# Optimization experiments

Hardware: AMD Instinct MI355X
Metric: run time of the kernel (lower is better)

## Reference

```python
import jax, jax.numpy as jnp
import numpy as np
from jax import lax

# ---- dims ----
B, L, DM = 4, 1024, 512          # batch, seq_len, model_dimension
NLAYERS = 6
EXPAND, HEADDIM, NSTATE, DCONV = 2, 64, 16, 4   # Mamba2 defaults; d_state = hidden_state_dim
DI = EXPAND * DM                 # d_inner = 1024
NH = DI // HEADDIM               # nheads = 16
CONV_DIM = DI + 2 * NSTATE       # x,B,C channels through depthwise conv = 1056
DPROJ = 2 * DI + 2 * NSTATE + NH # in_proj output width = 2096
DFF = 2048
EPS = 1e-5


def rmsnorm(x, w):
    return x * lax.rsqrt(jnp.mean(x * x, axis=-1, keepdims=True) + EPS) * w


def setup_inputs() -> dict:
    key = jax.random.key(0)
    ks = jax.random.split(key, 10)
    s = 0.02
    Ly = NLAYERS
    return {
        "x": jax.random.normal(ks[0], (B, L, DM), jnp.float32),
        "in_proj_w": jax.random.normal(ks[1], (Ly, DPROJ, DM), jnp.float32) * s,
        "conv_w": jax.random.normal(ks[2], (Ly, CONV_DIM, DCONV), jnp.float32) * s,
        "conv_b": jnp.zeros((Ly, CONV_DIM), jnp.float32),
        "dt_bias": jax.random.normal(ks[3], (Ly, NH), jnp.float32) * 0.5,
        "A_log": jnp.log(jax.random.uniform(ks[4], (Ly, NH), jnp.float32, 1.0, 16.0)),
        "D_ssm": jnp.ones((Ly, NH), jnp.float32),
        "gnorm_w": jnp.ones((Ly, DI), jnp.float32),
        "out_proj_w": jax.random.normal(ks[5], (Ly, DM, DI), jnp.float32) * s,
        "ffn_w1": jax.random.normal(ks[6], (Ly, DFF, DM), jnp.float32) * s,
        "ffn_b1": jnp.zeros((Ly, DFF), jnp.float32),
        "ffn_w2": jax.random.normal(ks[7], (Ly, DM, DFF), jnp.float32) * s,
        "ffn_b2": jnp.zeros((Ly, DM), jnp.float32),
        "norm_mamba_w": jnp.ones((Ly, DM), jnp.float32),
        "norm_ffn_w": jnp.ones((Ly, DM), jnp.float32),
        "final_norm_w": jnp.ones((DM,), jnp.float32),
    }


def _mamba2(u, Wp, cw, cb, dtb, Alog, Dh, gw, Wo):
    b, l, _ = u.shape
    zxbcdt = u @ Wp.T                                  # [b,l,DPROJ]
    z = zxbcdt[..., :DI]                               # gate
    xBC = zxbcdt[..., DI:DI + CONV_DIM]
    dt = jax.nn.softplus(zxbcdt[..., -NH:] + dtb)      # [b,l,H]
    # causal depthwise conv1d over time
    conv = lax.conv_general_dilated(
        xBC.transpose(0, 2, 1), cw[:, None, :], (1,), [(DCONV - 1, 0)],
        feature_group_count=CONV_DIM)
    xBC = jax.nn.silu(conv.transpose(0, 2, 1) + cb)
    xh = xBC[..., :DI].reshape(b, l, NH, HEADDIM)      # [b,l,H,P]
    Bm = xBC[..., DI:DI + NSTATE]                      # [b,l,N]
    Cm = xBC[..., DI + NSTATE:]                        # [b,l,N]
    dA = jnp.exp(dt * (-jnp.exp(Alog)))                # [b,l,H]

    def step(h, inp):
        xt, Bt, Ct, dAt, dtt = inp                     # [b,H,P],[b,N],[b,N],[b,H],[b,H]
        h = h * dAt[:, :, None, None] + (dtt[:, :, None] * xt)[..., None] * Bt[:, None, None, :]
        return h, jnp.einsum('bhpn,bn->bhp', h, Ct)

    h0 = jnp.zeros((b, NH, HEADDIM, NSTATE), u.dtype)
    xs = tuple(jnp.moveaxis(a, 1, 0) for a in (xh, Bm, Cm, dA, dt))
    _, ys = lax.scan(step, h0, xs)                     # ys: [l,b,H,P]
    y = jnp.moveaxis(ys, 0, 1) + Dh[None, None, :, None] * xh
    y = y.reshape(b, l, DI)
    y = rmsnorm(y * jax.nn.silu(z), gw)                # RMSNormGated
    return y @ Wo.T


def reference(x, in_proj_w, conv_w, conv_b, dt_bias, A_log, D_ssm, gnorm_w,
              out_proj_w, ffn_w1, ffn_b1, ffn_w2, ffn_b2,
              norm_mamba_w, norm_ffn_w, final_norm_w):
    for i in range(NLAYERS):
        res = x
        xn = rmsnorm(x, norm_mamba_w[i])
        x = _mamba2(xn, in_proj_w[i], conv_w[i], conv_b[i], dt_bias[i],
                    A_log[i], D_ssm[i], gnorm_w[i], out_proj_w[i]) + res
        res = x
        xn = rmsnorm(x, norm_ffn_w[i])
        h = jax.nn.gelu(xn @ ffn_w1[i].T + ffn_b1[i], approximate=False)
        x = h @ ffn_w2[i].T + ffn_b2[i] + res
    return rmsnorm(x, final_norm_w)
```

## Files before the change

### kernel.cpp

```cpp
#include <hip/hip_runtime.h>
#include <hip/hip_bf16.h>

#define NLAYERS 6
#define B_ 4
#define L_ 1024
#define DM_ 512
#define DI_ 1024
#define NH_ 16
#define HD_ 64
#define NS_ 16
#define CONVD_ 1056
#define DPROJ_ 2096
#define DFF_ 2048
#define ROWS_ (B_*L_)
#define EPS_ 1e-5f
#define NCHUNK_ 16
#define CLEN_ 64

typedef __bf16 bfx8 __attribute__((ext_vector_type(8)));
typedef float f32x4 __attribute__((ext_vector_type(4)));

typedef unsigned int u32_t;
typedef __attribute__((address_space(1))) const u32_t gu32_t;
typedef __attribute__((address_space(3))) u32_t lu32_t;

__device__ __forceinline__ void gload16(const __bf16* g, __bf16* l){
    __builtin_amdgcn_global_load_lds((gu32_t*)g, (lu32_t*)l, 16, 0, 0);
}

__device__ __forceinline__ float block_reduce_sum(float v){
    __shared__ float sm[8];
    #pragma unroll
    for (int off = 32; off > 0; off >>= 1) v += __shfl_xor(v, off);
    int lane = threadIdx.x & 63, wid = threadIdx.x >> 6;
    if (lane == 0) sm[wid] = v;
    __syncthreads();
    if (threadIdx.x == 0){
        float t = 0.f;
        int nw = blockDim.x >> 6;
        for (int i = 0; i < nw; i++) t += sm[i];
        sm[0] = t;
    }
    __syncthreads();
    return sm[0];
}

__global__ void copy_kernel(const float* __restrict__ x, float* __restrict__ X, int n){
    int i = blockIdx.x * blockDim.x + threadIdx.x;
    if (i < n) X[i] = x[i];
}

__global__ __launch_bounds__(64) void rowscale_kernel(const float* __restrict__ X,
                                                      float* __restrict__ rs){
    int row = blockIdx.x, lane = threadIdx.x;
    const float* xr = X + (size_t)row * DM_;
    float ss = 0.f;
    #pragma unroll
    for (int i = 0; i < DM_ / 64; i++){ float v = xr[lane + 64 * i]; ss += v * v; }
    #pragma unroll
    for (int off = 32; off > 0; off >>= 1) ss += __shfl_xor(ss, off);
    if (lane == 0) rs[row] = rsqrtf(ss / (float)DM_ + EPS_);
}

__global__ void finalnorm_kernel(const float* __restrict__ in, const float* __restrict__ w,
                                 float* __restrict__ out){
    int row = blockIdx.x;
    const float* xr = in + (size_t)row * DM_;
    float ss = 0.f;
    for (int c = threadIdx.x; c < DM_; c += blockDim.x){ float v = xr[c]; ss += v * v; }
    float tot = block_reduce_sum(ss);
    float rsv = rsqrtf(tot / (float)DM_ + EPS_);
    float* orow = out + (size_t)row * DM_;
    for (int c = threadIdx.x; c < DM_; c += blockDim.x)
        orow[c] = xr[c] * rsv * w[c];
}

__global__ void convA_kernel(const float* __restrict__ X, int lda,
                             const float* __restrict__ rs, const float* __restrict__ wv,
                             __bf16* __restrict__ A2, int M, int K){
    int idx = blockIdx.x * blockDim.x + threadIdx.x;
    if (idx >= M * K) return;
    int m = idx / K, k = idx - m * K;
    float a = X[(size_t)m * lda + k];
    if (rs) a *= rs[m];
    if (wv) a *= wv[k];
    __bf16 hi = (__bf16)a;
    A2[(size_t)m * (2 * K) + k] = hi;
    A2[(size_t)m * (2 * K) + K + k] = (__bf16)(a - (float)hi);
}

__global__ void convW_kernel(const float* __restrict__ W, __bf16* __restrict__ W2,
                             int N, int Npad, int K){
    int idx = blockIdx.x * blockDim.x + threadIdx.x;
    if (idx >= Npad * K) return;
    int n = idx / K, k = idx - n * K;
    size_t ro = (size_t)n * (3 * K);
    if (n >= N){
        W2[ro + k] = (__bf16)0.f; W2[ro + K + k] = (__bf16)0.f; W2[ro + 2 * K + k] = (__bf16)0.f;
        return;
    }
    float w = W[(size_t)n * K + k];
    __bf16 hi = (__bf16)w;
    __bf16 lo = (__bf16)(w - (float)hi);
    W2[ro + k] = hi; W2[ro + K + k] = lo; W2[ro + 2 * K + k] = hi;
}

__global__ void reduceK_kernel(const float* __restrict__ P, const float* __restrict__ bias,
                               float* __restrict__ X, int MN){
    int i = blockIdx.x * blockDim.x + threadIdx.x;
    if (i * 4 >= MN) return;
    float4 a = reinterpret_cast<const float4*>(P)[i];
    float4 b = reinterpret_cast<const float4*>(P + MN)[i];
    float4 x = reinterpret_cast<const float4*>(X)[i];
    float4 r;
    r.x = x.x + a.x + b.x; r.y = x.y + a.y + b.y;
    r.z = x.z + a.z + b.z; r.w = x.w + a.w + b.w;
    if (bias){
        int n = (i * 4) & (DM_ - 1);
        r.x += bias[n]; r.y += bias[n + 1]; r.z += bias[n + 2]; r.w += bias[n + 3];
    }
    reinterpret_cast<float4*>(X)[i] = r;
}

template<int BM, int BN>
__global__ __launch_bounds__(256, 3) void gemm_mfma_kernel(
    const __bf16* __restrict__ A2, const __bf16* __restrict__ W2,
    const float* __restrict__ bias, const float* __restrict__ resid, int ldr,
    float* __restrict__ Pf,
    float* __restrict__ Cf, int ldc, __bf16* __restrict__ Cs, int csK,
    int M, int N, int K, int act)
{
    constexpr int NI  = BM / 32;
    constexpr int NJ  = BN / 32;
    constexpr int NLD = (BM + BN) / 64;
    __shared__ __attribute__((aligned(16))) __bf16 As[3][BM * 32];
    __shared__ __attribute__((aligned(16))) __bf16 Ws[3][BN * 32];
    int tid = threadIdx.x;
    int m0 = blockIdx.x * BM, n0 = blockIdx.y * BN;
    int wv = tid >> 6, lane = tid & 63;
    int wm = (wv >> 1) * (BM / 2);
    int wn = (wv & 1) * (BN / 2);
    int lm = lane & 15, quad = lane >> 4;
    int soff = ((quad ^ ((lm >> 1) & 3)) * 8);
    const int ldA = 2 * K, ldW = 3 * K;
    const int nt = (3 * K) / 32;
    const int ntl = nt / gridDim.z;
    const int tb = blockIdx.z * ntl;

    f32x4 acc[NI][NJ] = {};

    auto stage = [&](int buf, int t){
        int k0 = t * 32;
        int ak0 = (k0 < K) ? k0 : (k0 - K);
        #pragma unroll
        for (int u = 0; u < BM / 64; u++){
            int cb = (wv * (BM / 64) + u) * 64;
            int c = cb + lane;
            int r = c >> 2, s = c & 3, q = s ^ ((r >> 1) & 3);
            gload16(A2 + (size_t)(m0 + r) * ldA + ak0 + q * 8, &As[buf][cb * 8]);
        }
        #pragma unroll
        for (int u = 0; u < BN / 64; u++){
            int cb = (wv * (BN / 64) + u) * 64;
            int c = cb + lane;
            int r = c >> 2, s = c & 3, q = s ^ ((r >> 1) & 3);
            gload16(W2 + (size_t)(n0 + r) * ldW + k0 + q * 8, &Ws[buf][cb * 8]);
        }
    };

    stage(0, tb);
    stage(1, tb + 1);
    if constexpr (NLD == 4)      asm volatile("s_waitcnt vmcnt(4)" ::: "memory");
    else if constexpr (NLD == 3) asm volatile("s_waitcnt vmcnt(3)" ::: "memory");
    else                         asm volatile("s_waitcnt vmcnt(2)" ::: "memory");
    __builtin_amdgcn_s_barrier();

    int cur = 0;
    for (int tt = 0; tt < ntl; tt++){
        bool staged = (tt + 2 < ntl);
        if (staged){
            int nb = cur + 2; if (nb >= 3) nb -= 3;
            stage(nb, tb + tt + 2);
        }

        bfx8 af[NI], bfr[NJ];
        #pragma unroll
        for (int i = 0; i < NI; i++)
            af[i] = *reinterpret_cast<const bfx8*>(&As[cur][(wm + i * 16 + lm) * 32 + soff]);
        #pragma unroll
        for (int j = 0; j < NJ; j++)
            bfr[j] = *reinterpret_cast<const bfx8*>(&Ws[cur][(wn + j * 16 + lm) * 32 + soff]);

        __builtin_amdgcn_s_setprio(1);
        #pragma unroll
        for (int i = 0; i < NI; i++)
            #pragma unroll
            for (int j = 0; j < NJ; j++)
                acc[i][j] = __builtin_amdgcn_mfma_f32_16x16x32_bf16(
                    af[i], bfr[j], acc[i][j], 0, 0, 0);
        __builtin_amdgcn_s_setprio(0);

        if (staged){
            if constexpr (NLD == 4)      asm volatile("s_waitcnt vmcnt(4)" ::: "memory");
            else if constexpr (NLD == 3) asm volatile("s_waitcnt vmcnt(3)" ::: "memory");
            else                         asm volatile("s_waitcnt vmcnt(2)" ::: "memory");
        } else {
            asm volatile("s_waitcnt vmcnt(0)" ::: "memory");
        }
        __builtin_amdgcn_s_barrier();
        cur = cur + 1; if (cur >= 3) cur = 0;
    }

    if (Pf){
        float* pc = Pf + (size_t)blockIdx.z * M * N;
        #pragma unroll
        for (int i = 0; i < NI; i++)
            #pragma unroll
            for (int j = 0; j < NJ; j++){
                int n = n0 + wn + j * 16 + lm;
                #pragma unroll
                for (int r = 0; r < 4; r++){
                    int m = m0 + wm + i * 16 + quad * 4 + r;
                    pc[(size_t)m * N + n] = acc[i][j][r];
                }
            }
        return;
    }

    #pragma unroll
    for (int i = 0; i < NI; i++){
        #pragma unroll
        for (int j = 0; j < NJ; j++){
            int n = n0 + wn + j * 16 + lm;
            if (n < N){
                #pragma unroll
                for (int r = 0; r < 4; r++){
                    int m = m0 + wm + i * 16 + quad * 4 + r;
                    float c = acc[i][j][r];
                    if (bias) c += bias[n];
                    if (act == 1) c = 0.5f * c * (1.f + erff(c * 0.70710678118654752f));
                    if (resid) c += resid[(size_t)m * ldr + n];
                    if (Cf) Cf[(size_t)m * ldc + n] = c;
                    else {
                        __bf16 hi = (__bf16)c;
                        Cs[(size_t)m * (2 * csK) + n] = hi;
                        Cs[(size_t)m * (2 * csK) + csK + n] = (__bf16)(c - (float)hi);
                    }
                }
            }
        }
    }
}

__global__ void bcconv_kernel(const float* __restrict__ ZX, const float* __restrict__ cw,
                              const float* __restrict__ cb, float* __restrict__ BCc){
    int idx = blockIdx.x * blockDim.x + threadIdx.x;
    if (idx >= ROWS_ * 32) return;
    int j = idx & 31;
    int row = idx >> 5;
    int l = row & (L_ - 1);
    float acc = cb[DI_ + j];
    #pragma unroll
    for (int k = 0; k < 4; k++){
        int lt = l + k - 3;
        if (lt >= 0)
            acc += ZX[(size_t)(row + k - 3) * DPROJ_ + (DI_ + DI_) + j] * cw[(DI_ + j) * 4 + k];
    }
    BCc[idx] = acc / (1.f + expf(-acc));
}

__global__ void dt_kernel(const float* __restrict__ ZX, const float* __restrict__ dtb,
                          const float* __restrict__ Alog, float* __restrict__ DT,
                          float* __restrict__ DA){
    int idx = blockIdx.x * blockDim.x + threadIdx.x;
    if (idx >= ROWS_ * NH_) return;
    int h = idx & 15; int row = idx >> 4;
    float v = ZX[(size_t)row * DPROJ_ + (DPROJ_ - NH_) + h] + dtb[h];
    float dtv = (v > 20.f) ? v : log1pf(expf(v));
    DT[idx] = dtv;
    DA[idx] = expf(-expf(Alog[h]) * dtv);
}

__global__ __launch_bounds__(64) void scanA_kernel(const float* __restrict__ ZX,
                                                   const float* __restrict__ BCc,
                                                   const float* __restrict__ DT,
                                                   const float* __restrict__ DA,
                                                   const float* __restrict__ cw,
                                                   const float* __restrict__ cb,
                                                   float* __restrict__ SCH,
                                                   float* __restrict__ PCH,
                                                   float* __restrict__ XWIN){
    int blk = blockIdx.x;
    int c = blk & (NCHUNK_ - 1); int h = (blk >> 4) & (NH_ - 1); int b = blk >> 8;
    int p = threadIdx.x;
    int ch = h * HD_ + p;
    float cw0 = cw[ch * 4 + 0], cw1 = cw[ch * 4 + 1], cw2 = cw[ch * 4 + 2], cw3 = cw[ch * 4 + 3];
    float cbc = cb[ch];
    size_t colx = (size_t)DI_ + ch;
    int t0 = c * CLEN_;
    float w0 = 0.f, w1 = 0.f, w2 = 0.f;
    if (c > 0){
        w0 = ZX[(size_t)(b * L_ + t0 - 3) * DPROJ_ + colx];
        w1 = ZX[(size_t)(b * L_ + t0 - 2) * DPROJ_ + colx];
        w2 = ZX[(size_t)(b * L_ + t0 - 1) * DPROJ_ + colx];
    }
    float* xw = XWIN + (size_t)blk * (3 * 64);
    xw[0 * 64 + p] = w0; xw[1 * 64 + p] = w1; xw[2 * 64 + p] = w2;

    float s[16];
    #pragma unroll
    for (int n = 0; n < 16; n++) s[n] = 0.f;
    float pprod = 1.f;

    for (int tt = 0; tt < CLEN_; tt++){
        int row = b * L_ + t0 + tt;
        size_t rowoff = (size_t)row * DPROJ_;
        float cur = ZX[rowoff + colx];
        float pre = cbc + cw0 * w0 + cw1 * w1 + cw2 * w2 + cw3 * cur;
        float xc = pre / (1.f + expf(-pre));
        w0 = w1; w1 = w2; w2 = cur;
        float dtv = DT[row * NH_ + h];
        float dav = DA[row * NH_ + h];
        pprod *= dav;
        float bc[16];
        const float4* bp = reinterpret_cast<const float4*>(BCc + (size_t)row * 32);
        #pragma unroll
        for (int i = 0; i < 4; i++){
            float4 v = bp[i];
            bc[4 * i + 0] = v.x; bc[4 * i + 1] = v.y; bc[4 * i + 2] = v.z; bc[4 * i + 3] = v.w;
        }
        float coef = dtv * xc;
        #pragma unroll
        for (int n = 0; n < 16; n++)
            s[n] = fmaf(s[n], dav, coef * bc[n]);
    }
    float* sc = SCH + (size_t)blk * 1024 + p * 16;
    #pragma unroll
    for (int i = 0; i < 4; i++)
        *reinterpret_cast<float4*>(sc + 4 * i) = make_float4(s[4*i], s[4*i+1], s[4*i+2], s[4*i+3]);
    if (p == 0) PCH[blk] = pprod;
}

__global__ __launch_bounds__(64) void scanB_kernel(float* __restrict__ SCH,
                                                   const float* __restrict__ PCH){
    int bh = blockIdx.x;
    int p = threadIdx.x;
    float s[16];
    #pragma unroll
    for (int n = 0; n < 16; n++) s[n] = 0.f;
    for (int c = 0; c < NCHUNK_; c++){
        int blk = bh * NCHUNK_ + c;
        float* sc = SCH + (size_t)blk * 1024 + p * 16;
        float loc[16];
        #pragma unroll
        for (int i = 0; i < 4; i++){
            float4 v = *reinterpret_cast<const float4*>(sc + 4 * i);
            loc[4*i] = v.x; loc[4*i+1] = v.y; loc[4*i+2] = v.z; loc[4*i+3] = v.w;
        }
        float P = PCH[blk];
        #pragma unroll
        for (int i = 0; i < 4; i++)
            *reinterpret_cast<float4*>(sc + 4 * i) = make_float4(s[4*i], s[4*i+1], s[4*i+2], s[4*i+3]);
        #pragma unroll
        for (int n = 0; n < 16; n++)
            s[n] = fmaf(P, s[n], loc[n]);
    }
}

__global__ __launch_bounds__(64) void scanC_kernel(float* __restrict__ ZX,
                                                   const float* __restrict__ BCc,
                                                   const float* __restrict__ DT,
                                                   const float* __restrict__ DA,
                                                   const float* __restrict__ cw,
                                                   const float* __restrict__ cb,
                                                   const float* __restrict__ Dh,
                                                   const float* __restrict__ SCH,
                                                   const float* __restrict__ XWIN){
    int blk = blockIdx.x;
    int c = blk & (NCHUNK_ - 1); int h = (blk >> 4) & (NH_ - 1); int b = blk >> 8;
    int p = threadIdx.x;
    int ch = h * HD_ + p;
    float cw0 = cw[ch * 4 + 0], cw1 = cw[ch * 4 + 1], cw2 = cw[ch * 4 + 2], cw3 = cw[ch * 4 + 3];
    float cbc = cb[ch];
    float Dv = Dh[h];
    size_t colx = (size_t)DI_ + ch;
    int t0 = c * CLEN_;
    const float* xw = XWIN + (size_t)blk * (3 * 64);
    float w0 = xw[0 * 64 + p], w1 = xw[1 * 64 + p], w2 = xw[2 * 64 + p];
    const float* sc = SCH + (size_t)blk * 1024 + p * 16;
    float s[16];
    #pragma unroll
    for (int i = 0; i < 4; i++){
        float4 v = *reinterpret_cast<const float4*>(sc + 4 * i);
        s[4*i] = v.x; s[4*i+1] = v.y; s[4*i+2] = v.z; s[4*i+3] = v.w;
    }

    for (int tt = 0; tt < CLEN_; tt++){
        int row = b * L_ + t0 + tt;
        size_t rowoff = (size_t)row * DPROJ_;
        float cur = ZX[rowoff + colx];
        float pre = cbc + cw0 * w0 + cw1 * w1 + cw2 * w2 + cw3 * cur;
        float xc = pre / (1.f + expf(-pre));
        w0 = w1; w1 = w2; w2 = cur;
        float dtv = DT[row * NH_ + h];
        float dav = DA[row * NH_ + h];
        float bc[32];
        const float4* bp = reinterpret_cast<const float4*>(BCc + (size_t)row * 32);
        #pragma unroll
        for (int i = 0; i < 8; i++){
            float4 v = bp[i];
            bc[4 * i + 0] = v.x; bc[4 * i + 1] = v.y; bc[4 * i + 2] = v.z; bc[4 * i + 3] = v.w;
        }
        float coef = dtv * xc;
        float y = 0.f;
        #pragma unroll
        for (int n = 0; n < 16; n++){
            s[n] = fmaf(s[n], dav, coef * bc[n]);
            y += s[n] * bc[16 + n];
        }
        ZX[rowoff + colx] = fmaf(Dv, xc, y);
    }
}

__global__ void gatenorm_kernel(float* __restrict__ ZX, const float* __restrict__ gw){
    int row = blockIdx.x;
    float* zr = ZX + (size_t)row * DPROJ_;
    float* yr = zr + DI_;
    float ss = 0.f;
    for (int cc = threadIdx.x; cc < DI_; cc += blockDim.x){
        float z = zr[cc];
        float v = yr[cc] * (z / (1.f + expf(-z)));
        yr[cc] = v;
        ss += v * v;
    }
    float tot = block_reduce_sum(ss);
    float rsv = rsqrtf(tot / (float)DI_ + EPS_);
    for (int cc = threadIdx.x; cc < DI_; cc += blockDim.x)
        yr[cc] = yr[cc] * rsv * gw[cc];
}

extern "C" void kernel_launch(void* const* d_in, const int* in_sizes, int n_in,
                              void* d_out, int out_size, void* d_ws, size_t ws_size,
                              hipStream_t stream){
    const float* x_in        = (const float*)d_in[0];
    const float* in_proj_w   = (const float*)d_in[1];
    const float* conv_w      = (const float*)d_in[2];
    const float* conv_b      = (const float*)d_in[3];
    const float* dt_bias     = (const float*)d_in[4];
    const float* A_log       = (const float*)d_in[5];
    const float* D_ssm       = (const float*)d_in[6];
    const float* gnorm_w     = (const float*)d_in[7];
    const float* out_proj_w  = (const float*)d_in[8];
    const float* ffn_w1      = (const float*)d_in[9];
    const float* ffn_b1      = (const float*)d_in[10];
    const float* ffn_w2      = (const float*)d_in[11];
    const float* ffn_b2      = (const float*)d_in[12];
    const float* norm_mamba_w= (const float*)d_in[13];
    const float* norm_ffn_w  = (const float*)d_in[14];
    const float* final_norm_w= (const float*)d_in[15];

    float* X    = (float*)d_ws;
    float* RS   = X    + 2097152;
    float* BCc  = RS   + 4096;
    float* DT   = BCc  + 131072;
    float* DA   = DT   + 65536;
    float* SCH  = DA   + 65536;
    float* PCH  = SCH  + 1048576;
    float* XWIN = PCH  + 1024;
    __bf16* A2  = (__bf16*)(XWIN + 196608);
    __bf16* W2  = A2 + 8388608;
    float* ZX   = (float*)(W2 + 3342336);
    __bf16* Hs  = (__bf16*)ZX;
    float* PART_OP = ZX;
    float* PART_F2 = (float*)A2;

    const int NBLK = B_ * NH_ * NCHUNK_;

    copy_kernel<<<(ROWS_ * DM_ + 255) / 256, 256, 0, stream>>>(x_in, X, ROWS_ * DM_);

    for (int l = 0; l < NLAYERS; l++){
        const float* cwl = conv_w + (size_t)l * CONVD_ * 4;
        const float* cbl = conv_b + (size_t)l * CONVD_;

        rowscale_kernel<<<ROWS_, 64, 0, stream>>>(X, RS);
        convA_kernel<<<(ROWS_ * DM_ + 255) / 256, 256, 0, stream>>>(
            X, DM_, RS, norm_mamba_w + (size_t)l * DM_, A2, ROWS_, DM_);
        convW_kernel<<<(2176 * DM_ + 255) / 256, 256, 0, stream>>>(
            in_proj_w + (size_t)l * DPROJ_ * DM_, W2, DPROJ_, 2176, DM_);
        {
            dim3 g(ROWS_ / 128, 2176 / 128, 1);
            gemm_mfma_kernel<128,128><<<g, 256, 0, stream>>>(A2, W2, nullptr, nullptr, 0,
                                                             nullptr, ZX, DPROJ_, nullptr, 0,
                                                             ROWS_, DPROJ_, DM_, 0);
        }

        bcconv_kernel<<<(ROWS_ * 32 + 255) / 256, 256, 0, stream>>>(ZX, cwl, cbl, BCc);
        dt_kernel<<<(ROWS_ * NH_ + 255) / 256, 256, 0, stream>>>(
            ZX, dt_bias + (size_t)l * NH_, A_log + (size_t)l * NH_, DT, DA);

        scanA_kernel<<<NBLK, 64, 0, stream>>>(ZX, BCc, DT, DA, cwl, cbl, SCH, PCH, XWIN);
        scanB_kernel<<<B_ * NH_, 64, 0, stream>>>(SCH, PCH);
        scanC_kernel<<<NBLK, 64, 0, stream>>>(ZX, BCc, DT, DA, cwl, cbl,
                                              D_ssm + (size_t)l * NH_, SCH, XWIN);

        gatenorm_kernel<<<ROWS_, 256, 0, stream>>>(ZX, gnorm_w + (size_t)l * DI_);

        convA_kernel<<<(ROWS_ * DI_ + 255) / 256, 256, 0, stream>>>(
            ZX + DI_, DPROJ_, nullptr, nullptr, A2, ROWS_, DI_);
        convW_kernel<<<(DM_ * DI_ + 255) / 256, 256, 0, stream>>>(
            out_proj_w + (size_t)l * DM_ * DI_, W2, DM_, DM_, DI_);
        {
            dim3 g(ROWS_ / 64, DM_ / 64, 2);
            gemm_mfma_kernel<64,64><<<g, 256, 0, stream>>>(A2, W2, nullptr, nullptr, 0,
                                                           PART_OP, nullptr, 0, nullptr, 0,
                                                           ROWS_, DM_, DI_, 0);
        }
        reduceK_kernel<<<(ROWS_ * DM_ / 4 + 255) / 256, 256, 0, stream>>>(
            PART_OP, nullptr, X, ROWS_ * DM_);

        rowscale_kernel<<<ROWS_, 64, 0, stream>>>(X, RS);
        convA_kernel<<<(ROWS_ * DM_ + 255) / 256, 256, 0, stream>>>(
            X, DM_, RS, norm_ffn_w + (size_t)l * DM_, A2, ROWS_, DM_);
        convW_kernel<<<(DFF_ * DM_ + 255) / 256, 256, 0, stream>>>(
            ffn_w1 + (size_t)l * DFF_ * DM_, W2, DFF_, DFF_, DM_);
        {
            dim3 g(ROWS_ / 128, DFF_ / 128, 1);
            gemm_mfma_kernel<128,128><<<g, 256, 0, stream>>>(A2, W2, ffn_b1 + (size_t)l * DFF_,
                                                             nullptr, 0, nullptr,
                                                             nullptr, 0, Hs, DFF_,
                                                             ROWS_, DFF_, DM_, 1);
        }
        convW_kernel<<<(DM_ * DFF_ + 255) / 256, 256, 0, stream>>>(
            ffn_w2 + (size_t)l * DM_ * DFF_, W2, DM_, DM_, DFF_);
        {
            dim3 g(ROWS_ / 64, DM_ / 64, 2);
            gemm_mfma_kernel<64,64><<<g, 256, 0, stream>>>(Hs, W2, nullptr, nullptr, 0,
                                                           PART_F2, nullptr, 0, nullptr, 0,
                                                           ROWS_, DM_, DFF_, 0);
        }
        reduceK_kernel<<<(ROWS_ * DM_ / 4 + 255) / 256, 256, 0, stream>>>(
            PART_F2, ffn_b2 + (size_t)l * DM_, X, ROWS_ * DM_);
    }

    finalnorm_kernel<<<ROWS_, 256, 0, stream>>>(X, final_norm_w, (float*)d_out);
}
```

Baseline: 2.068 ms.

## Reuse hi/lo split tiles across three MFMA products and remap blocks per XCD

The split-bf16 GEMM used to stream a 3K-long concatenated K axis (hi, lo, hi of W against hi/lo of A). It now loads the hi and lo halves of both A and W once per 32-wide K chunk and issues hi*hi, hi*lo and lo*hi MFMAs from registers. This drops the duplicated W hi copy and the extra global-to-LDS traffic. The grid becomes 1D with a mapping that sends tiles sharing an N-tile to the same XCD for L2 reuse, and the large GEMMs switch to 128x64 tiles with per-tile occupancy bounds. LDS use per block doubles and register pressure rises.

```diff
diff --git a/kernel.cpp b/kernel.cpp
--- a/kernel.cpp
+++ b/kernel.cpp
@@ -94,15 +94,15 @@
     int idx = blockIdx.x * blockDim.x + threadIdx.x;
     if (idx >= Npad * K) return;
     int n = idx / K, k = idx - n * K;
-    size_t ro = (size_t)n * (3 * K);
+    size_t ro = (size_t)n * (2 * K);
     if (n >= N){
-        W2[ro + k] = (__bf16)0.f; W2[ro + K + k] = (__bf16)0.f; W2[ro + 2 * K + k] = (__bf16)0.f;
+        W2[ro + k] = (__bf16)0.f; W2[ro + K + k] = (__bf16)0.f;
         return;
     }
     float w = W[(size_t)n * K + k];
     __bf16 hi = (__bf16)w;
     __bf16 lo = (__bf16)(w - (float)hi);
-    W2[ro + k] = hi; W2[ro + K + k] = lo; W2[ro + 2 * K + k] = hi;
+    W2[ro + k] = hi; W2[ro + K + k] = lo;
 }
 
 __global__ void reduceK_kernel(const float* __restrict__ P, const float* __restrict__ bias,
@@ -123,56 +123,66 @@
 }
 
 template<int BM, int BN>
-__global__ __launch_bounds__(256, 3) void gemm_mfma_kernel(
+__global__ __launch_bounds__(256, (BM == 64) ? 3 : 2) void gemm_mfma_kernel(
     const __bf16* __restrict__ A2, const __bf16* __restrict__ W2,
     const float* __restrict__ bias, const float* __restrict__ resid, int ldr,
     float* __restrict__ Pf,
     float* __restrict__ Cf, int ldc, __bf16* __restrict__ Cs, int csK,
-    int M, int N, int K, int act)
+    int M, int N, int K, int act, int NTM, int NTN)
 {
-    constexpr int NI  = BM / 32;
-    constexpr int NJ  = BN / 32;
-    constexpr int NLD = (BM + BN) / 64;
-    __shared__ __attribute__((aligned(16))) __bf16 As[3][BM * 32];
-    __shared__ __attribute__((aligned(16))) __bf16 Ws[3][BN * 32];
+    constexpr int WTM = BM / 2, WTN = BN / 2;
+    constexpr int NI  = WTM / 16;
+    constexpr int NJ  = WTN / 16;
+    constexpr int NLD = (BM + BN) / 32;
+    constexpr int AH  = BM * 32;
+    constexpr int WH  = BN * 32;
+    __shared__ __attribute__((aligned(16))) __bf16 As[3][2 * AH];
+    __shared__ __attribute__((aligned(16))) __bf16 Ws[3][2 * WH];
+    int bid = blockIdx.x;
+    int xcd = bid & 7, li = bid >> 3;
+    int mt = li % NTM, g = li / NTM;
+    int ntile = g * 8 + xcd;
+    if (ntile >= NTN) return;
+    int m0 = mt * BM, n0 = ntile * BN;
     int tid = threadIdx.x;
-    int m0 = blockIdx.x * BM, n0 = blockIdx.y * BN;
     int wv = tid >> 6, lane = tid & 63;
-    int wm = (wv >> 1) * (BM / 2);
-    int wn = (wv & 1) * (BN / 2);
+    int wm = (wv >> 1) * WTM;
+    int wn = (wv & 1) * WTN;
     int lm = lane & 15, quad = lane >> 4;
     int soff = ((quad ^ ((lm >> 1) & 3)) * 8);
-    const int ldA = 2 * K, ldW = 3 * K;
-    const int nt = (3 * K) / 32;
-    const int ntl = nt / gridDim.z;
+    const int ldA = 2 * K, ldW = 2 * K;
+    const int nchunk = K / 32;
+    const int ntl = nchunk / gridDim.z;
     const int tb = blockIdx.z * ntl;
 
     f32x4 acc[NI][NJ] = {};
 
     auto stage = [&](int buf, int t){
-        int k0 = t * 32;
-        int ak0 = (k0 < K) ? k0 : (k0 - K);
+        int kc = t * 32;
         #pragma unroll
         for (int u = 0; u < BM / 64; u++){
             int cb = (wv * (BM / 64) + u) * 64;
             int c = cb + lane;
             int r = c >> 2, s = c & 3, q = s ^ ((r >> 1) & 3);
-            gload16(A2 + (size_t)(m0 + r) * ldA + ak0 + q * 8, &As[buf][cb * 8]);
+            const __bf16* ga = A2 + (size_t)(m0 + r) * ldA + kc + q * 8;
+            gload16(ga,     &As[buf][cb * 8]);
+            gload16(ga + K, &As[buf][AH + cb * 8]);
         }
         #pragma unroll
         for (int u = 0; u < BN / 64; u++){
             int cb = (wv * (BN / 64) + u) * 64;
             int c = cb + lane;
             int r = c >> 2, s = c & 3, q = s ^ ((r >> 1) & 3);
-            gload16(W2 + (size_t)(n0 + r) * ldW + k0 + q * 8, &Ws[buf][cb * 8]);
+            const __bf16* gw = W2 + (size_t)(n0 + r) * ldW + kc + q * 8;
+            gload16(gw,     &Ws[buf][cb * 8]);
+            gload16(gw + K, &Ws[buf][WH + cb * 8]);
         }
     };
 
     stage(0, tb);
     stage(1, tb + 1);
-    if constexpr (NLD == 4)      asm volatile("s_waitcnt vmcnt(4)" ::: "memory");
-    else if constexpr (NLD == 3) asm volatile("s_waitcnt vmcnt(3)" ::: "memory");
-    else                         asm volatile("s_waitcnt vmcnt(2)" ::: "memory");
+    if constexpr (NLD == 6) asm volatile("s_waitcnt vmcnt(6)" ::: "memory");
+    else                    asm volatile("s_waitcnt vmcnt(4)" ::: "memory");
     __builtin_amdgcn_s_barrier();
 
     int cur = 0;
@@ -183,13 +193,19 @@
             stage(nb, tb + tt + 2);
         }
 
-        bfx8 af[NI], bfr[NJ];
-        #pragma unroll
-        for (int i = 0; i < NI; i++)
-            af[i] = *reinterpret_cast<const bfx8*>(&As[cur][(wm + i * 16 + lm) * 32 + soff]);
-        #pragma unroll
-        for (int j = 0; j < NJ; j++)
-            bfr[j] = *reinterpret_cast<const bfx8*>(&Ws[cur][(wn + j * 16 + lm) * 32 + soff]);
+        bfx8 ah[NI], al[NI], bh[NJ], bl[NJ];
+        #pragma unroll
+        for (int i = 0; i < NI; i++){
+            int ra = (wm + i * 16 + lm) * 32 + soff;
+            ah[i] = *reinterpret_cast<const bfx8*>(&As[cur][ra]);
+            al[i] = *reinterpret_cast<const bfx8*>(&As[cur][AH + ra]);
+        }
+        #pragma unroll
+        for (int j = 0; j < NJ; j++){
+            int rb = (wn + j * 16 + lm) * 32 + soff;
+            bh[j] = *reinterpret_cast<const bfx8*>(&Ws[cur][rb]);
+            bl[j] = *reinterpret_cast<const bfx8*>(&Ws[cur][WH + rb]);
+        }
 
         __builtin_amdgcn_s_setprio(1);
         #pragma unroll
@@ -197,13 +213,24 @@
             #pragma unroll
             for (int j = 0; j < NJ; j++)
                 acc[i][j] = __builtin_amdgcn_mfma_f32_16x16x32_bf16(
-                    af[i], bfr[j], acc[i][j], 0, 0, 0);
+                    ah[i], bh[j], acc[i][j], 0, 0, 0);
+        #pragma unroll
+        for (int i = 0; i < NI; i++)
+            #pragma unroll
+            for (int j = 0; j < NJ; j++)
+                acc[i][j] = __builtin_amdgcn_mfma_f32_16x16x32_bf16(
+                    ah[i], bl[j], acc[i][j], 0, 0, 0);
+        #pragma unroll
+        for (int i = 0; i < NI; i++)
+            #pragma unroll
+            for (int j = 0; j < NJ; j++)
+                acc[i][j] = __builtin_amdgcn_mfma_f32_16x16x32_bf16(
+                    al[i], bh[j], acc[i][j], 0, 0, 0);
         __builtin_amdgcn_s_setprio(0);
 
         if (staged){
-            if constexpr (NLD == 4)      asm volatile("s_waitcnt vmcnt(4)" ::: "memory");
-            else if constexpr (NLD == 3) asm volatile("s_waitcnt vmcnt(3)" ::: "memory");
-            else                         asm volatile("s_waitcnt vmcnt(2)" ::: "memory");
+            if constexpr (NLD == 6) asm volatile("s_waitcnt vmcnt(6)" ::: "memory");
+            else                    asm volatile("s_waitcnt vmcnt(4)" ::: "memory");
         } else {
             asm volatile("s_waitcnt vmcnt(0)" ::: "memory");
         }
@@ -488,10 +515,9 @@
         convW_kernel<<<(2176 * DM_ + 255) / 256, 256, 0, stream>>>(
             in_proj_w + (size_t)l * DPROJ_ * DM_, W2, DPROJ_, 2176, DM_);
         {
-            dim3 g(ROWS_ / 128, 2176 / 128, 1);
-            gemm_mfma_kernel<128,128><<<g, 256, 0, stream>>>(A2, W2, nullptr, nullptr, 0,
-                                                             nullptr, ZX, DPROJ_, nullptr, 0,
-                                                             ROWS_, DPROJ_, DM_, 0);
+            gemm_mfma_kernel<128,64><<<dim3(1280,1,1), 256, 0, stream>>>(
+                A2, W2, nullptr, nullptr, 0, nullptr,
+                ZX, DPROJ_, nullptr, 0, ROWS_, DPROJ_, DM_, 0, 32, 34);
         }
 
         bcconv_kernel<<<(ROWS_ * 32 + 255) / 256, 256, 0, stream>>>(ZX, cwl, cbl, BCc);
@@ -510,10 +536,9 @@
         convW_kernel<<<(DM_ * DI_ + 255) / 256, 256, 0, stream>>>(
             out_proj_w + (size_t)l * DM_ * DI_, W2, DM_, DM_, DI_);
         {
-            dim3 g(ROWS_ / 64, DM_ / 64, 2);
-            gemm_mfma_kernel<64,64><<<g, 256, 0, stream>>>(A2, W2, nullptr, nullptr, 0,
-                                                           PART_OP, nullptr, 0, nullptr, 0,
-                                                           ROWS_, DM_, DI_, 0);
+            gemm_mfma_kernel<64,64><<<dim3(512,1,2), 256, 0, stream>>>(
+                A2, W2, nullptr, nullptr, 0, PART_OP,
+                nullptr, 0, nullptr, 0, ROWS_, DM_, DI_, 0, 64, 8);
         }
         reduceK_kernel<<<(ROWS_ * DM_ / 4 + 255) / 256, 256, 0, stream>>>(
             PART_OP, nullptr, X, ROWS_ * DM_);
@@ -524,19 +549,16 @@
         convW_kernel<<<(DFF_ * DM_ + 255) / 256, 256, 0, stream>>>(
             ffn_w1 + (size_t)l * DFF_ * DM_, W2, DFF_, DFF_, DM_);
         {
-            dim3 g(ROWS_ / 128, DFF_ / 128, 1);
-            gemm_mfma_kernel<128,128><<<g, 256, 0, stream>>>(A2, W2, ffn_b1 + (size_t)l * DFF_,
-                                                             nullptr, 0, nullptr,
-                                                             nullptr, 0, Hs, DFF_,
-                                                             ROWS_, DFF_, DM_, 1);
+            gemm_mfma_kernel<128,64><<<dim3(1024,1,1), 256, 0, stream>>>(
+                A2, W2, ffn_b1 + (size_t)l * DFF_, nullptr, 0, nullptr,
+                nullptr, 0, Hs, DFF_, ROWS_, DFF_, DM_, 1, 32, 32);
         }
         convW_kernel<<<(DM_ * DFF_ + 255) / 256, 256, 0, stream>>>(
             ffn_w2 + (size_t)l * DM_ * DFF_, W2, DM_, DM_, DFF_);
         {
-            dim3 g(ROWS_ / 64, DM_ / 64, 2);
-            gemm_mfma_kernel<64,64><<<g, 256, 0, stream>>>(Hs, W2, nullptr, nullptr, 0,
-                                                           PART_F2, nullptr, 0, nullptr, 0,
-                                                           ROWS_, DM_, DFF_, 0);
+            gemm_mfma_kernel<64,64><<<dim3(512,1,2), 256, 0, stream>>>(
+                Hs, W2, nullptr, nullptr, 0, PART_F2,
+                nullptr, 0, nullptr, 0, ROWS_, DM_, DFF_, 0, 64, 8);
         }
         reduceK_kernel<<<(ROWS_ * DM_ / 4 + 255) / 256, 256, 0, stream>>>(
             PART_F2, ffn_b2 + (size_t)l * DM_, X, ROWS_ * DM_);
```

Measured after the change: 2.170 ms. 4.9% more time.
